# Performance work log

Hardware: AMD Instinct MI355X
Metric: run time of the kernel (lower is better)

## Reference

```python
import jax, jax.numpy as jnp
import numpy as np

K_SIZE = 5      # kernel_size
NUM_ITERS = 3   # num_iters
EPS = 1e-6


def _unfold(x, k):
    """Mimic F.unfold(x, k, padding=k//2) -> (B, N, K, D) with K=k*k, N=H*W.
    Channel ordering matches torch: unfold gives (B, D*K, N) with d-major, so
    view(B, D, K, N).permute(0, 3, 2, 1) == transpose below."""
    B, D, H, W = x.shape
    p = k // 2
    xp = jnp.pad(x, ((0, 0), (0, 0), (p, p), (p, p)))
    # stack k*k shifted views -> (B, D, K, H, W); loop is over the fixed 5x5 window
    patches = jnp.stack([xp[:, :, i:i + H, j:j + W]
                         for i in range(k) for j in range(k)], axis=2)
    return patches.reshape(B, D, k * k, H * W).transpose(0, 3, 2, 1)  # (B,N,K,D)


def setup_inputs() -> dict:
    key = jax.random.key(0)
    embeddings = jax.random.normal(key, (2, 32, 256, 256), dtype=jnp.float32)
    # init_bandwidth=1.0 -> log(exp(1)-1) so softplus(log_bandwidth)=1.0
    log_bandwidth = jnp.asarray(np.log(np.exp(1.0) - 1.0), dtype=jnp.float32)
    return {"embeddings": embeddings, "log_bandwidth": log_bandwidth}


def reference(embeddings, log_bandwidth):
    B, D, H, W = embeddings.shape
    N = H * W
    z = embeddings.reshape(B, D, N).transpose(0, 2, 1)  # (B, N, D)
    bandwidth = jax.nn.softplus(log_bandwidth)
    inv_2bw2 = 1.0 / (2.0 * bandwidth * bandwidth)
    # NOTE: original code unfolds `embeddings` (not z) every iter -> constant patches
    patches = _unfold(embeddings, K_SIZE)  # (B, N, K, D)
    for _ in range(NUM_ITERS):
        z_flat = jax.lax.stop_gradient(z)  # matches z.detach()
        diff = patches - z_flat[:, :, None, :]           # (B, N, K, D)
        dist2 = jnp.sum(diff * diff, axis=-1)            # (B, N, K)
        weights = jnp.exp(-dist2 * inv_2bw2)             # gaussian kernel
        numerator = jnp.einsum('bnk,bnkd->bnd', weights, patches)
        denom = jnp.sum(weights, axis=2, keepdims=True) + EPS
        z = numerator / denom
    # default flags: only shifted embeddings are returned
    return z.transpose(0, 2, 1).reshape(B, D, H, W)
```

## Files before the change

### kernel.cpp

```cpp
#include <hip/hip_runtime.h>
#include <math.h>


typedef _Float16 h2  __attribute__((ext_vector_type(2)));
typedef unsigned int u4v __attribute__((ext_vector_type(4)));

constexpr int Dch  = 32;
constexpr int HH   = 256;
constexpr int WW   = 256;
constexpr int PADp = 2;
constexpr int BH   = 16;
constexpr int BW   = 16;
constexpr int THs  = 20;
constexpr int RSTR = 25;
constexpr int PSTR = THs * RSTR + 1;
constexpr int NJOB = 4 * THs * 6;
constexpr int ITERS = 3;
constexpr int HWp  = HH * WW;
constexpr int NTHR = 512;

__device__ __forceinline__ float fdot2f(h2 a, h2 b, float c) {
    return __builtin_amdgcn_fdot2(a, b, c, false);
}

__device__ __forceinline__ float EXP2F(float x) {
#if __has_builtin(__builtin_amdgcn_exp2f)
    return __builtin_amdgcn_exp2f(x);
#else
    return __expf(x * 0.69314718055994531f);
#endif
}

__device__ __forceinline__ float qswap(float x) {
#if __has_builtin(__builtin_amdgcn_mov_dpp)
    return __int_as_float(
        __builtin_amdgcn_mov_dpp(__float_as_int(x), 0xB1, 0xF, 0xF, true));
#else
    return __shfl_xor(x, 1, 64);
#endif
}

__device__ __forceinline__ h2 as_h2(unsigned int x) {
    return __builtin_bit_cast(h2, x);
}

__device__ __forceinline__ h2 pk2(float a, float b) {
#if __has_builtin(__builtin_amdgcn_cvt_pkrtz)
    return __builtin_bit_cast(h2, __builtin_amdgcn_cvt_pkrtz(a, b));
#else
    h2 r; r[0] = (_Float16)a; r[1] = (_Float16)b; return r;
#endif
}

__device__ __forceinline__ unsigned int pku(float a, float b) {
    return __builtin_bit_cast(unsigned int, pk2(a, b));
}

__global__ __launch_bounds__(NTHR, 4)
void meanshift_kernel(const float* __restrict__ E,
                      const float* __restrict__ lbw,
                      float* __restrict__ out)
{
    __shared__ u4v  tile[4 * PSTR];
    __shared__ float sqv[THs * RSTR];

    const int bz  = blockIdx.z;
    const int oh  = blockIdx.y * BH - PADp;
    const int owc = blockIdx.x * BW;
    const int gw0 = owc - 4;
    const int tid = threadIdx.x;
    const int half = tid & 1;
    const int pix  = tid >> 1;
    const int px   = pix & (BW - 1);
    const int py   = pix >> 4;
    const int c0   = 2 * half;

    const float bwv = log1pf(__expf(lbw[0]));
    const float cc2 = 1.0f / (2.0f * bwv * bwv);
    const float NCf = cc2 * 1.44269504f;
    const float A2f = 2.0f * NCf;
    const float MZC = -1.0f / (8.0f * NCf);

    const float* Eb = E + (size_t)bz * Dch * HWp;

    if (tid < NJOB) {
        const int cc  = tid / (THs * 6);
        const int rem = tid - cc * (THs * 6);
        const int row = rem / 6;
        const int g   = rem - row * 6;
        const int gh  = oh + row;
        const int gwb = gw0 + 4 * g;

        float4 F0 = {0.f,0.f,0.f,0.f}, F1 = F0, F2 = F0, F3 = F0;
        float4 F4 = F0, F5 = F0, F6 = F0, F7 = F0;
        if ((unsigned)gh < (unsigned)HH) {
            const float* base = Eb + (size_t)(8 * cc) * HWp + gh * WW;
            if (gwb >= 0 && gwb + 4 <= WW) {
                F0 = *(const float4*)(base + 0 * (size_t)HWp + gwb);
                F1 = *(const float4*)(base + 1 * (size_t)HWp + gwb);
                F2 = *(const float4*)(base + 2 * (size_t)HWp + gwb);
                F3 = *(const float4*)(base + 3 * (size_t)HWp + gwb);
                F4 = *(const float4*)(base + 4 * (size_t)HWp + gwb);
                F5 = *(const float4*)(base + 5 * (size_t)HWp + gwb);
                F6 = *(const float4*)(base + 6 * (size_t)HWp + gwb);
                F7 = *(const float4*)(base + 7 * (size_t)HWp + gwb);
            } else {
                const bool i0 = (unsigned)(gwb + 0) < (unsigned)WW;
                const bool i1 = (unsigned)(gwb + 1) < (unsigned)WW;
                const bool i2 = (unsigned)(gwb + 2) < (unsigned)WW;
                const bool i3 = (unsigned)(gwb + 3) < (unsigned)WW;
#define GE(K) F##K = make_float4( \
                    i0 ? base[(K) * (size_t)HWp + gwb + 0] : 0.f, \
                    i1 ? base[(K) * (size_t)HWp + gwb + 1] : 0.f, \
                    i2 ? base[(K) * (size_t)HWp + gwb + 2] : 0.f, \
                    i3 ? base[(K) * (size_t)HWp + gwb + 3] : 0.f)
                GE(0); GE(1); GE(2); GE(3); GE(4); GE(5); GE(6); GE(7);
#undef GE
            }
        }
        const int wbase = cc * PSTR + row * RSTR + 4 * g;
        u4v W;
        W[0]=pku(F0.x,F1.x); W[1]=pku(F2.x,F3.x); W[2]=pku(F4.x,F5.x); W[3]=pku(F6.x,F7.x);
        tile[wbase + 0] = W;
        W[0]=pku(F0.y,F1.y); W[1]=pku(F2.y,F3.y); W[2]=pku(F4.y,F5.y); W[3]=pku(F6.y,F7.y);
        tile[wbase + 1] = W;
        W[0]=pku(F0.z,F1.z); W[1]=pku(F2.z,F3.z); W[2]=pku(F4.z,F5.z); W[3]=pku(F6.z,F7.z);
        tile[wbase + 2] = W;
        W[0]=pku(F0.w,F1.w); W[1]=pku(F2.w,F3.w); W[2]=pku(F4.w,F5.w); W[3]=pku(F6.w,F7.w);
        tile[wbase + 3] = W;
    }
    __syncthreads();

    if (tid < THs * 24) {
        const int row = tid / 24;
        const int col = tid - row * 24;
        const int p   = row * RSTR + col;
        const u4v t0 = tile[0 * PSTR + p], t1 = tile[1 * PSTR + p];
        const u4v t2 = tile[2 * PSTR + p], t3 = tile[3 * PSTR + p];
        float a0 = 0.f, a1 = 0.f, a2 = 0.f, a3 = 0.f;
        #pragma unroll
        for (int j = 0; j < 4; ++j) {
            const h2 q0 = as_h2(t0[j]); a0 = fdot2f(q0, q0, a0);
            const h2 q1 = as_h2(t1[j]); a1 = fdot2f(q1, q1, a1);
            const h2 q2 = as_h2(t2[j]); a2 = fdot2f(q2, q2, a2);
            const h2 q3 = as_h2(t3[j]); a3 = fdot2f(q3, q3, a3);
        }
        sqv[p] = -0.5f * NCf * ((a0 + a1) + (a2 + a3));
    }
    __syncthreads();

    const u4v* __restrict__ tA = tile + c0 * PSTR;
    const u4v* __restrict__ tB = tA + PSTR;

    h2 zs0, zs1, zs2, zs3, zs4, zs5, zs6, zs7;
    {
        const int myp = (py + 2) * RSTR + (px + 4);
        const u4v ca = tA[myp];
        const u4v cb = tB[myp];
        const h2 A2v = pk2(A2f, A2f);
        zs0 = as_h2(ca[0]) * A2v; zs1 = as_h2(ca[1]) * A2v;
        zs2 = as_h2(ca[2]) * A2v; zs3 = as_h2(ca[3]) * A2v;
        zs4 = as_h2(cb[0]) * A2v; zs5 = as_h2(cb[1]) * A2v;
        zs6 = as_h2(cb[2]) * A2v; zs7 = as_h2(cb[3]) * A2v;
    }

    float* Ob = out + (size_t)bz * Dch * HWp;
    const int off    = (oh + PADp + py) * WW + (owc + px);
    const int chbase = 16 * half;

#define NBODY(NPI) do {                                                       \
        const u4v a  = tA[(NPI)];                                             \
        const u4v bq = tB[(NPI)];                                             \
        const float Sv = sqv[(NPI)];                                          \
        const h2 pa0 = as_h2(a[0]),  pa1 = as_h2(a[1]);                       \
        const h2 pa2 = as_h2(a[2]),  pa3 = as_h2(a[3]);                       \
        const h2 pb0 = as_h2(bq[0]), pb1 = as_h2(bq[1]);                      \
        const h2 pb2 = as_h2(bq[2]), pb3 = as_h2(bq[3]);                      \
        float s0 = fdot2f(pa0, zs0, Sv);                                      \
        s0 = fdot2f(pa1, zs1, s0); s0 = fdot2f(pa2, zs2, s0);                 \
        s0 = fdot2f(pa3, zs3, s0);                                            \
        float s1 = fdot2f(pb0, zs4, mzz);                                     \
        s1 = fdot2f(pb1, zs5, s1); s1 = fdot2f(pb2, zs6, s1);                 \
        s1 = fdot2f(pb3, zs7, s1);                                            \
        const float dp  = s0 + s1;                                            \
        const float arg = dp + qswap(dp);     \
        const float w   = EXP2F(arg);                              \
        den += w;                                                             \
        const h2 w2v = pk2(w, w);                                             \
        n0 += pa0 * w2v; n1 += pa1 * w2v; n2 += pa2 * w2v; n3 += pa3 * w2v;   \
        n4 += pb0 * w2v; n5 += pb1 * w2v; n6 += pb2 * w2v; n7 += pb3 * w2v;   \
    } while (0)

    #pragma unroll 1
    for (int it = 0; it < ITERS; ++it) {
        float mzz;
        {
            float q0 = fdot2f(zs0, zs0, 0.f);
            q0 = fdot2f(zs1, zs1, q0); q0 = fdot2f(zs2, zs2, q0);
            q0 = fdot2f(zs3, zs3, q0);
            float q1 = fdot2f(zs4, zs4, 0.f);
            q1 = fdot2f(zs5, zs5, q1); q1 = fdot2f(zs6, zs6, q1);
            q1 = fdot2f(zs7, zs7, q1);
            const float qs = q0 + q1;
            mzz = (qs + qswap(qs)) * MZC;
        }

        h2 n0 = {(_Float16)0.f, (_Float16)0.f};
        h2 n1 = n0, n2 = n0, n3 = n0, n4 = n0, n5 = n0, n6 = n0, n7 = n0;
        float den = 0.f;

        #pragma unroll 1
        for (int di = 0; di < 5; ++di) {
            const int rb = (py + di) * RSTR + px + 2;
            NBODY(rb + 0);
            NBODY(rb + 1);
            NBODY(rb + 2);
            NBODY(rb + 3);
            NBODY(rb + 4);
        }

        const float invf = 1.0f / (den + 1e-6f);
        if (it == ITERS - 1) {
#define WR(IDX, NV, EL) Ob[(size_t)(chbase + (IDX)) * HWp + off] = (float)NV[EL] * invf
            WR(0,  n0, 0); WR(1,  n0, 1); WR(2,  n1, 0); WR(3,  n1, 1);
            WR(4,  n2, 0); WR(5,  n2, 1); WR(6,  n3, 0); WR(7,  n3, 1);
            WR(8,  n4, 0); WR(9,  n4, 1); WR(10, n5, 0); WR(11, n5, 1);
            WR(12, n6, 0); WR(13, n6, 1); WR(14, n7, 0); WR(15, n7, 1);
#undef WR
        } else {
            const float ia = invf * A2f;
            const h2 iv = pk2(ia, ia);
            zs0 = n0 * iv; zs1 = n1 * iv; zs2 = n2 * iv; zs3 = n3 * iv;
            zs4 = n4 * iv; zs5 = n5 * iv; zs6 = n6 * iv; zs7 = n7 * iv;
        }
    }
#undef NBODY
}

extern "C" void kernel_launch(void* const* d_in, const int* in_sizes, int n_in,
                              void* d_out, int out_size, void* d_ws, size_t ws_size,
                              hipStream_t stream) {
    const float* E   = (const float*)d_in[0];
    const float* lbw = (const float*)d_in[1];
    float* out       = (float*)d_out;

    const int B = in_sizes[0] / (Dch * HWp);
    dim3 grid(WW / BW, HH / BH, B);
    dim3 block(NTHR, 1, 1);
    hipLaunchKernelGGL(meanshift_kernel, grid, block, 0, stream, E, lbw, out);
}
```

Before: 31.21 us.

## Compute two vertically adjacent pixels per thread to reuse window loads

Each thread pair now handles two pixels stacked vertically instead of one. A 6-row sweep loads each neighbour once from LDS and applies it to both pixels, cutting LDS reads per pixel. The block tile grows to 32x16 output pixels with a 36-row halo, the fill loops become strided, and the occupancy hint drops to 2. In exchange, register pressure roughly doubles with two sets of accumulators and there are half as many blocks, which may reduce occupancy and latency hiding.

New measurement: 34.59 us. +10.8%, slower.

```diff
diff --git a/kernel.cpp b/kernel.cpp
--- a/kernel.cpp
+++ b/kernel.cpp
@@ -8,10 +8,9 @@
 constexpr int Dch  = 32;
 constexpr int HH   = 256;
 constexpr int WW   = 256;
-constexpr int PADp = 2;
-constexpr int BH   = 16;
+constexpr int BH   = 32;
 constexpr int BW   = 16;
-constexpr int THs  = 20;
+constexpr int THs  = 36;
 constexpr int RSTR = 25;
 constexpr int PSTR = THs * RSTR + 1;
 constexpr int NJOB = 4 * THs * 6;
@@ -56,7 +55,7 @@
     return __builtin_bit_cast(unsigned int, pk2(a, b));
 }
 
-__global__ __launch_bounds__(NTHR, 4)
+__global__ __launch_bounds__(NTHR, 2)
 void meanshift_kernel(const float* __restrict__ E,
                       const float* __restrict__ lbw,
                       float* __restrict__ out)
@@ -65,14 +64,15 @@
     __shared__ float sqv[THs * RSTR];
 
     const int bz  = blockIdx.z;
-    const int oh  = blockIdx.y * BH - PADp;
+    const int oh  = blockIdx.y * BH - 2;
     const int owc = blockIdx.x * BW;
     const int gw0 = owc - 4;
     const int tid = threadIdx.x;
     const int half = tid & 1;
-    const int pix  = tid >> 1;
-    const int px   = pix & (BW - 1);
-    const int py   = pix >> 4;
+    const int pr   = tid >> 1;
+    const int px   = pr & (BW - 1);
+    const int pyy  = pr >> 4;
+    const int py0  = 2 * pyy;
     const int c0   = 2 * half;
 
     const float bwv = log1pf(__expf(lbw[0]));
@@ -83,9 +83,9 @@
 
     const float* Eb = E + (size_t)bz * Dch * HWp;
 
-    if (tid < NJOB) {
-        const int cc  = tid / (THs * 6);
-        const int rem = tid - cc * (THs * 6);
+    for (int job = tid; job < NJOB; job += NTHR) {
+        const int cc  = job / (THs * 6);
+        const int rem = job - cc * (THs * 6);
         const int row = rem / 6;
         const int g   = rem - row * 6;
         const int gh  = oh + row;
@@ -131,9 +131,9 @@
     }
     __syncthreads();
 
-    if (tid < THs * 24) {
-        const int row = tid / 24;
-        const int col = tid - row * 24;
+    for (int q = tid; q < THs * 24; q += NTHR) {
+        const int row = q / 24;
+        const int col = q - row * 24;
         const int p   = row * RSTR + col;
         const u4v t0 = tile[0 * PSTR + p], t1 = tile[1 * PSTR + p];
         const u4v t2 = tile[2 * PSTR + p], t3 = tile[3 * PSTR + p];
@@ -152,89 +152,144 @@
     const u4v* __restrict__ tA = tile + c0 * PSTR;
     const u4v* __restrict__ tB = tA + PSTR;
 
-    h2 zs0, zs1, zs2, zs3, zs4, zs5, zs6, zs7;
+    h2 zA0, zA1, zA2, zA3, zA4, zA5, zA6, zA7;
+    h2 zB0, zB1, zB2, zB3, zB4, zB5, zB6, zB7;
     {
-        const int myp = (py + 2) * RSTR + (px + 4);
-        const u4v ca = tA[myp];
-        const u4v cb = tB[myp];
+        const int mypA = (py0 + 2) * RSTR + (px + 4);
+        const int mypB = mypA + RSTR;
         const h2 A2v = pk2(A2f, A2f);
-        zs0 = as_h2(ca[0]) * A2v; zs1 = as_h2(ca[1]) * A2v;
-        zs2 = as_h2(ca[2]) * A2v; zs3 = as_h2(ca[3]) * A2v;
-        zs4 = as_h2(cb[0]) * A2v; zs5 = as_h2(cb[1]) * A2v;
-        zs6 = as_h2(cb[2]) * A2v; zs7 = as_h2(cb[3]) * A2v;
+        const u4v ca = tA[mypA], cb = tB[mypA];
+        zA0 = as_h2(ca[0]) * A2v; zA1 = as_h2(ca[1]) * A2v;
+        zA2 = as_h2(ca[2]) * A2v; zA3 = as_h2(ca[3]) * A2v;
+        zA4 = as_h2(cb[0]) * A2v; zA5 = as_h2(cb[1]) * A2v;
+        zA6 = as_h2(cb[2]) * A2v; zA7 = as_h2(cb[3]) * A2v;
+        const u4v da = tA[mypB], db = tB[mypB];
+        zB0 = as_h2(da[0]) * A2v; zB1 = as_h2(da[1]) * A2v;
+        zB2 = as_h2(da[2]) * A2v; zB3 = as_h2(da[3]) * A2v;
+        zB4 = as_h2(db[0]) * A2v; zB5 = as_h2(db[1]) * A2v;
+        zB6 = as_h2(db[2]) * A2v; zB7 = as_h2(db[3]) * A2v;
     }
 
     float* Ob = out + (size_t)bz * Dch * HWp;
-    const int off    = (oh + PADp + py) * WW + (owc + px);
+    const int offA   = (oh + 2 + py0) * WW + (owc + px);
     const int chbase = 16 * half;
 
-#define NBODY(NPI) do {                                                       \
-        const u4v a  = tA[(NPI)];                                             \
-        const u4v bq = tB[(NPI)];                                             \
-        const float Sv = sqv[(NPI)];                                          \
-        const h2 pa0 = as_h2(a[0]),  pa1 = as_h2(a[1]);                       \
-        const h2 pa2 = as_h2(a[2]),  pa3 = as_h2(a[3]);                       \
-        const h2 pb0 = as_h2(bq[0]), pb1 = as_h2(bq[1]);                      \
-        const h2 pb2 = as_h2(bq[2]), pb3 = as_h2(bq[3]);                      \
-        float s0 = fdot2f(pa0, zs0, Sv);                                      \
-        s0 = fdot2f(pa1, zs1, s0); s0 = fdot2f(pa2, zs2, s0);                 \
-        s0 = fdot2f(pa3, zs3, s0);                                            \
-        float s1 = fdot2f(pb0, zs4, mzz);                                     \
-        s1 = fdot2f(pb1, zs5, s1); s1 = fdot2f(pb2, zs6, s1);                 \
-        s1 = fdot2f(pb3, zs7, s1);                                            \
+#define NB(PA0,PA1,PA2,PA3,PB0,PB1,PB2,PB3, SV, ZP, NP, DEN, MZZ) do {        \
+        float s0 = fdot2f(PA0, ZP##0, (SV));                                  \
+        s0 = fdot2f(PA1, ZP##1, s0); s0 = fdot2f(PA2, ZP##2, s0);             \
+        s0 = fdot2f(PA3, ZP##3, s0);                                          \
+        float s1 = fdot2f(PB0, ZP##4, (MZZ));                                 \
+        s1 = fdot2f(PB1, ZP##5, s1); s1 = fdot2f(PB2, ZP##6, s1);             \
+        s1 = fdot2f(PB3, ZP##7, s1);                                          \
         const float dp  = s0 + s1;                                            \
-        const float arg = dp + qswap(dp);     \
-        const float w   = EXP2F(arg);                              \
-        den += w;                                                             \
+        const float arg = dp + qswap(dp);                                     \
+        const float w   = EXP2F(arg);                                         \
+        DEN += w;                                                             \
         const h2 w2v = pk2(w, w);                                             \
-        n0 += pa0 * w2v; n1 += pa1 * w2v; n2 += pa2 * w2v; n3 += pa3 * w2v;   \
-        n4 += pb0 * w2v; n5 += pb1 * w2v; n6 += pb2 * w2v; n7 += pb3 * w2v;   \
+        NP##0 += PA0 * w2v; NP##1 += PA1 * w2v;                               \
+        NP##2 += PA2 * w2v; NP##3 += PA3 * w2v;                               \
+        NP##4 += PB0 * w2v; NP##5 += PB1 * w2v;                               \
+        NP##6 += PB2 * w2v; NP##7 += PB3 * w2v;                               \
     } while (0)
 
     #pragma unroll 1
     for (int it = 0; it < ITERS; ++it) {
-        float mzz;
+        float mzzA, mzzB;
         {
-            float q0 = fdot2f(zs0, zs0, 0.f);
-            q0 = fdot2f(zs1, zs1, q0); q0 = fdot2f(zs2, zs2, q0);
-            q0 = fdot2f(zs3, zs3, q0);
-            float q1 = fdot2f(zs4, zs4, 0.f);
-            q1 = fdot2f(zs5, zs5, q1); q1 = fdot2f(zs6, zs6, q1);
-            q1 = fdot2f(zs7, zs7, q1);
-            const float qs = q0 + q1;
-            mzz = (qs + qswap(qs)) * MZC;
-        }
-
-        h2 n0 = {(_Float16)0.f, (_Float16)0.f};
-        h2 n1 = n0, n2 = n0, n3 = n0, n4 = n0, n5 = n0, n6 = n0, n7 = n0;
-        float den = 0.f;
+            float q0 = fdot2f(zA0, zA0, 0.f);
+            q0 = fdot2f(zA1, zA1, q0); q0 = fdot2f(zA2, zA2, q0);
+            q0 = fdot2f(zA3, zA3, q0);
+            float q1 = fdot2f(zA4, zA4, 0.f);
+            q1 = fdot2f(zA5, zA5, q1); q1 = fdot2f(zA6, zA6, q1);
+            q1 = fdot2f(zA7, zA7, q1);
+            const float qa = q0 + q1;
+            mzzA = (qa + qswap(qa)) * MZC;
+            float r0 = fdot2f(zB0, zB0, 0.f);
+            r0 = fdot2f(zB1, zB1, r0); r0 = fdot2f(zB2, zB2, r0);
+            r0 = fdot2f(zB3, zB3, r0);
+            float r1 = fdot2f(zB4, zB4, 0.f);
+            r1 = fdot2f(zB5, zB5, r1); r1 = fdot2f(zB6, zB6, r1);
+            r1 = fdot2f(zB7, zB7, r1);
+            const float qb = r0 + r1;
+            mzzB = (qb + qswap(qb)) * MZC;
+        }
+
+        h2 nA0 = {(_Float16)0.f, (_Float16)0.f};
+        h2 nA1 = nA0, nA2 = nA0, nA3 = nA0, nA4 = nA0, nA5 = nA0, nA6 = nA0, nA7 = nA0;
+        h2 nB0 = nA0, nB1 = nA0, nB2 = nA0, nB3 = nA0, nB4 = nA0, nB5 = nA0, nB6 = nA0, nB7 = nA0;
+        float denA = 0.f, denB = 0.f;
 
         #pragma unroll 1
-        for (int di = 0; di < 5; ++di) {
-            const int rb = (py + di) * RSTR + px + 2;
-            NBODY(rb + 0);
-            NBODY(rb + 1);
-            NBODY(rb + 2);
-            NBODY(rb + 3);
-            NBODY(rb + 4);
-        }
-
-        const float invf = 1.0f / (den + 1e-6f);
+        for (int di = 0; di < 6; ++di) {
+            const int rw = (py0 + di) * RSTR + (px + 2);
+            const u4v qa0 = tA[rw+0], qa1 = tA[rw+1], qa2 = tA[rw+2];
+            const u4v qa3 = tA[rw+3], qa4 = tA[rw+4];
+            const u4v qb0 = tB[rw+0], qb1 = tB[rw+1], qb2 = tB[rw+2];
+            const u4v qb3 = tB[rw+3], qb4 = tB[rw+4];
+            const float S0 = sqv[rw+0], S1 = sqv[rw+1], S2 = sqv[rw+2];
+            const float S3 = sqv[rw+3], S4 = sqv[rw+4];
+#define EXPAND(Q) as_h2(Q[0]), as_h2(Q[1]), as_h2(Q[2]), as_h2(Q[3])
+            const h2 a00 = as_h2(qa0[0]), a01 = as_h2(qa0[1]), a02 = as_h2(qa0[2]), a03 = as_h2(qa0[3]);
+            const h2 a10 = as_h2(qa1[0]), a11 = as_h2(qa1[1]), a12 = as_h2(qa1[2]), a13 = as_h2(qa1[3]);
+            const h2 a20 = as_h2(qa2[0]), a21 = as_h2(qa2[1]), a22 = as_h2(qa2[2]), a23 = as_h2(qa2[3]);
+            const h2 a30 = as_h2(qa3[0]), a31 = as_h2(qa3[1]), a32 = as_h2(qa3[2]), a33 = as_h2(qa3[3]);
+            const h2 a40 = as_h2(qa4[0]), a41 = as_h2(qa4[1]), a42 = as_h2(qa4[2]), a43 = as_h2(qa4[3]);
+            const h2 b00 = as_h2(qb0[0]), b01 = as_h2(qb0[1]), b02 = as_h2(qb0[2]), b03 = as_h2(qb0[3]);
+            const h2 b10 = as_h2(qb1[0]), b11 = as_h2(qb1[1]), b12 = as_h2(qb1[2]), b13 = as_h2(qb1[3]);
+            const h2 b20 = as_h2(qb2[0]), b21 = as_h2(qb2[1]), b22 = as_h2(qb2[2]), b23 = as_h2(qb2[3]);
+            const h2 b30 = as_h2(qb3[0]), b31 = as_h2(qb3[1]), b32 = as_h2(qb3[2]), b33 = as_h2(qb3[3]);
+            const h2 b40 = as_h2(qb4[0]), b41 = as_h2(qb4[1]), b42 = as_h2(qb4[2]), b43 = as_h2(qb4[3]);
+#undef EXPAND
+            if (di != 5) {
+                NB(a00,a01,a02,a03, b00,b01,b02,b03, S0, zA, nA, denA, mzzA);
+                NB(a10,a11,a12,a13, b10,b11,b12,b13, S1, zA, nA, denA, mzzA);
+                NB(a20,a21,a22,a23, b20,b21,b22,b23, S2, zA, nA, denA, mzzA);
+                NB(a30,a31,a32,a33, b30,b31,b32,b33, S3, zA, nA, denA, mzzA);
+                NB(a40,a41,a42,a43, b40,b41,b42,b43, S4, zA, nA, denA, mzzA);
+            }
+            if (di != 0) {
+                NB(a00,a01,a02,a03, b00,b01,b02,b03, S0, zB, nB, denB, mzzB);
+                NB(a10,a11,a12,a13, b10,b11,b12,b13, S1, zB, nB, denB, mzzB);
+                NB(a20,a21,a22,a23, b20,b21,b22,b23, S2, zB, nB, denB, mzzB);
+                NB(a30,a31,a32,a33, b30,b31,b32,b33, S3, zB, nB, denB, mzzB);
+                NB(a40,a41,a42,a43, b40,b41,b42,b43, S4, zB, nB, denB, mzzB);
+            }
+        }
+
+        const float invA = 1.0f / (denA + 1e-6f);
+        const float invB = 1.0f / (denB + 1e-6f);
         if (it == ITERS - 1) {
-#define WR(IDX, NV, EL) Ob[(size_t)(chbase + (IDX)) * HWp + off] = (float)NV[EL] * invf
-            WR(0,  n0, 0); WR(1,  n0, 1); WR(2,  n1, 0); WR(3,  n1, 1);
-            WR(4,  n2, 0); WR(5,  n2, 1); WR(6,  n3, 0); WR(7,  n3, 1);
-            WR(8,  n4, 0); WR(9,  n4, 1); WR(10, n5, 0); WR(11, n5, 1);
-            WR(12, n6, 0); WR(13, n6, 1); WR(14, n7, 0); WR(15, n7, 1);
+#define WR(IDX, NV, EL, OFF, INV) \
+            Ob[(size_t)(chbase + (IDX)) * HWp + (OFF)] = (float)NV[EL] * (INV)
+            WR(0,  nA0, 0, offA, invA); WR(1,  nA0, 1, offA, invA);
+            WR(2,  nA1, 0, offA, invA); WR(3,  nA1, 1, offA, invA);
+            WR(4,  nA2, 0, offA, invA); WR(5,  nA2, 1, offA, invA);
+            WR(6,  nA3, 0, offA, invA); WR(7,  nA3, 1, offA, invA);
+            WR(8,  nA4, 0, offA, invA); WR(9,  nA4, 1, offA, invA);
+            WR(10, nA5, 0, offA, invA); WR(11, nA5, 1, offA, invA);
+            WR(12, nA6, 0, offA, invA); WR(13, nA6, 1, offA, invA);
+            WR(14, nA7, 0, offA, invA); WR(15, nA7, 1, offA, invA);
+            WR(0,  nB0, 0, offA + WW, invB); WR(1,  nB0, 1, offA + WW, invB);
+            WR(2,  nB1, 0, offA + WW, invB); WR(3,  nB1, 1, offA + WW, invB);
+            WR(4,  nB2, 0, offA + WW, invB); WR(5,  nB2, 1, offA + WW, invB);
+            WR(6,  nB3, 0, offA + WW, invB); WR(7,  nB3, 1, offA + WW, invB);
+            WR(8,  nB4, 0, offA + WW, invB); WR(9,  nB4, 1, offA + WW, invB);
+            WR(10, nB5, 0, offA + WW, invB); WR(11, nB5, 1, offA + WW, invB);
+            WR(12, nB6, 0, offA + WW, invB); WR(13, nB6, 1, offA + WW, invB);
+            WR(14, nB7, 0, offA + WW, invB); WR(15, nB7, 1, offA + WW, invB);
 #undef WR
         } else {
-            const float ia = invf * A2f;
-            const h2 iv = pk2(ia, ia);
-            zs0 = n0 * iv; zs1 = n1 * iv; zs2 = n2 * iv; zs3 = n3 * iv;
-            zs4 = n4 * iv; zs5 = n5 * iv; zs6 = n6 * iv; zs7 = n7 * iv;
+            const float iaA = invA * A2f;
+            const float iaB = invB * A2f;
+            const h2 ivA = pk2(iaA, iaA);
+            const h2 ivB = pk2(iaB, iaB);
+            zA0 = nA0 * ivA; zA1 = nA1 * ivA; zA2 = nA2 * ivA; zA3 = nA3 * ivA;
+            zA4 = nA4 * ivA; zA5 = nA5 * ivA; zA6 = nA6 * ivA; zA7 = nA7 * ivA;
+            zB0 = nB0 * ivB; zB1 = nB1 * ivB; zB2 = nB2 * ivB; zB3 = nB3 * ivB;
+            zB4 = nB4 * ivB; zB5 = nB5 * ivB; zB6 = nB6 * ivB; zB7 = nB7 * ivB;
         }
     }
-#undef NBODY
+#undef NB
 }
 
 extern "C" void kernel_launch(void* const* d_in, const int* in_sizes, int n_in,
```
